# Kernel tuning notes

Hardware: AMD Instinct MI355X
Metric: run time of the kernel (lower is better)

## Reference

```python
import jax, jax.numpy as jnp
import numpy as np

N_NODES = 100000
N_EDGES = 800000
F_IN, HID, N_CLS = 256, 128, 32


def setup_inputs() -> dict:
    key = jax.random.key(0)
    k1, k2, k3, k4, k5 = jax.random.split(key, 5)
    features = jax.random.normal(k1, (N_NODES, F_IN), dtype=jnp.float32)
    # random directed edges with no self loops (so add_remaining_self_loops == append all loops)
    src = jax.random.randint(k2, (N_EDGES,), 0, N_NODES)
    off = jax.random.randint(k3, (N_EDGES,), 1, N_NODES)
    dst = (src + off) % N_NODES
    edge_index = jnp.stack([src, dst]).astype(jnp.int64)
    # Glorot-style params for the two GCNConv layers
    W1 = jax.random.normal(k4, (F_IN, HID), dtype=jnp.float32) * (1.0 / np.sqrt(F_IN))
    b1 = jnp.zeros((HID,), dtype=jnp.float32)
    W2 = jax.random.normal(k5, (HID, N_CLS), dtype=jnp.float32) * (1.0 / np.sqrt(HID))
    b2 = jnp.zeros((N_CLS,), dtype=jnp.float32)
    return {"features": features, "edge_index": edge_index, "W1": W1, "b1": b1, "W2": W2, "b2": b2}


def _gcn_conv(x, W, b, src, dst, norm, n):
    xw = x @ W                                  # [N, d_out] dense GEMM
    msg = xw[src] * norm[:, None]               # gather + scale, [E, d_out]
    out = jax.ops.segment_sum(msg, dst, num_segments=n)  # scatter-add to targets
    return out + b


def reference(features, edge_index, W1, b1, W2, b2):
    n = features.shape[0]
    # add_remaining_self_loops (input has none, so append all)
    loops = jnp.arange(n, dtype=edge_index.dtype)
    src = jnp.concatenate([edge_index[0], loops])
    dst = jnp.concatenate([edge_index[1], loops])
    # gcn_norm: deg over targets, sym normalization deg^-1/2 A deg^-1/2
    deg = jax.ops.segment_sum(jnp.ones_like(src, dtype=features.dtype), dst, num_segments=n)
    dinv = jnp.where(deg > 0, jax.lax.rsqrt(deg), 0.0)
    norm = dinv[src] * dinv[dst]
    x = _gcn_conv(features, W1, b1, src, dst, norm, n)
    x = jax.nn.relu(x)
    # dropout is identity at inference (training=False)
    x = _gcn_conv(x, W2, b2, src, dst, norm, n)
    return jax.nn.log_softmax(x, axis=1)
```

## Files before the change

### kernel.cpp

```cpp
#include <hip/hip_runtime.h>
#include <hip/hip_bf16.h>

typedef __bf16 bf16_t;
typedef __attribute__((ext_vector_type(8))) __bf16 bf16x8;
typedef __attribute__((ext_vector_type(4))) float f32x4;
typedef __attribute__((ext_vector_type(2))) float f32x2;

__device__ inline int xcc_id() {
    int x;
    asm volatile("s_getreg_b32 %0, hwreg(20, 0, 32)" : "=s"(x));
    return x & 7;
}
__device__ inline int l2AtomicAdd(int* p, int v) {
    return __hip_atomic_fetch_add(p, v, __ATOMIC_RELAXED, __HIP_MEMORY_SCOPE_WORKGROUP);
}

__device__ inline void packB_one(const float* __restrict__ B, bf16_t* __restrict__ Bp,
                                 int N, int idx) {
    int j    = idx & 7;
    int lane = (idx >> 3) & 63;
    int st   = idx >> 9;
    int nt   = N >> 4;
    int s = st / nt, t = st - s * nt;
    int k = s * 32 + (lane >> 4) * 8 + j;
    int n = t * 16 + (lane & 15);
    Bp[idx] = (bf16_t)B[(size_t)k * N + n];
}

__device__ inline void fma8_fp8(uint2 u, float w, float* a) {
    f32x2 p;
    p = __builtin_amdgcn_cvt_pk_f32_fp8(u.x, false); a[0] += p[0] * w; a[1] += p[1] * w;
    p = __builtin_amdgcn_cvt_pk_f32_fp8(u.x, true);  a[2] += p[0] * w; a[3] += p[1] * w;
    p = __builtin_amdgcn_cvt_pk_f32_fp8(u.y, false); a[4] += p[0] * w; a[5] += p[1] * w;
    p = __builtin_amdgcn_cvt_pk_f32_fp8(u.y, true);  a[6] += p[0] * w; a[7] += p[1] * w;
}

__global__ __launch_bounds__(256) void k_prep(
        const float* __restrict__ W1, bf16_t* __restrict__ Bp1,
        const float* __restrict__ W2, bf16_t* __restrict__ Bp2,
        int* __restrict__ deg8, int n8) {
    int b = blockIdx.x, t = threadIdx.x;
    const int PACKB = (32768 + 4096) / 256;
    if (b < PACKB) {
        int idx = b * 256 + t;
        if (idx < 32768) packB_one(W1, Bp1, 128, idx);
        else             packB_one(W2, Bp2, 32, idx - 32768);
        return;
    }
    int i = ((b - PACKB) * 256 + t) * 4;
    if (i < n8) {
        if (i + 4 <= n8) *(int4*)(deg8 + i) = make_int4(0, 0, 0, 0);
        else for (int j = 0; i + j < n8; ++j) deg8[i + j] = 0;
    }
}

template <int KSTEPS, int NTILES>
__global__ __launch_bounds__(256) void k_front(
        const float* __restrict__ feat, const bf16_t* __restrict__ Bp1,
        unsigned char* __restrict__ XW1, int M,
        const int* __restrict__ dst, int* __restrict__ deg8,
        int* __restrict__ rank, int Nn, int E, int DEGB) {
    int b = blockIdx.x, t = threadIdx.x;
    if (b < DEGB) {
        int x = xcc_id();
        int* degx = deg8 + (size_t)x * Nn;
        int tag = x << 28;
        int i = b * 1024 + t * 4;
        if (i + 4 <= E) {
            int4 v = *(const int4*)(dst + i);
            int4 r;
            r.x = l2AtomicAdd(&degx[v.x], 1) | tag;
            r.y = l2AtomicAdd(&degx[v.y], 1) | tag;
            r.z = l2AtomicAdd(&degx[v.z], 1) | tag;
            r.w = l2AtomicAdd(&degx[v.w], 1) | tag;
            *(int4*)(rank + i) = r;
        } else {
            for (int j = 0; j < 4; ++j)
                if (i + j < E) rank[i + j] = l2AtomicAdd(&degx[dst[i + j]], 1) | tag;
        }
        return;
    }
    b -= DEGB;
    {
        int wave = (b * 256 + t) >> 6;
        if (wave * 16 >= M) return;
        int lane = t & 63;
        int r16 = lane & 15, quad = lane >> 4;
        const int K = KSTEPS * 32, N = NTILES * 16;
        f32x4 acc[NTILES] = {};
        const float* arow = feat + (size_t)(wave * 16 + r16) * K + quad * 8;
#pragma unroll
        for (int s = 0; s < KSTEPS; ++s) {
            const float* ap = arow + s * 32;
            bf16x8 a;
#pragma unroll
            for (int j = 0; j < 8; ++j) a[j] = (bf16_t)ap[j];
            const bf16_t* bp = Bp1 + ((size_t)(s * NTILES) * 64 + lane) * 8;
#pragma unroll
            for (int tt = 0; tt < NTILES; ++tt) {
                bf16x8 bb = *(const bf16x8*)(bp + tt * 512);
                acc[tt] = __builtin_amdgcn_mfma_f32_16x16x32_bf16(a, bb, acc[tt], 0, 0, 0);
            }
        }
#pragma unroll
        for (int tt = 0; tt < NTILES; ++tt)
#pragma unroll
            for (int r = 0; r < 4; ++r) {
                int pk = __builtin_amdgcn_cvt_pk_fp8_f32(acc[tt][r], acc[tt][r], 0, false);
                XW1[(size_t)(wave * 16 + quad * 4 + r) * N + tt * 16 + r16] =
                    (unsigned char)pk;
            }
    }
}

__global__ __launch_bounds__(256) void k_dinv_scan1(
        const int* __restrict__ deg8, int* __restrict__ degTot,
        int* __restrict__ off, float* __restrict__ dinv,
        int* __restrict__ bsum, int n) {
    __shared__ int red[256];
    int b = blockIdx.x, t = threadIdx.x;
    int base = b * 1024 + t * 4;
    int s = 0;
#pragma unroll
    for (int j = 0; j < 4; ++j) {
        int i = base + j;
        if (i < n) {
            int run = 0;
#pragma unroll
            for (int x = 0; x < 8; ++x) {
                int v = deg8[(size_t)x * n + i];
                off[(size_t)x * n + i] = run;
                run += v;
            }
            degTot[i] = run;
            s += run;
            dinv[i] = rsqrtf((float)(run + 1));
        }
    }
    red[t] = s;
    __syncthreads();
    for (int d = 128; d > 0; d >>= 1) {
        if (t < d) red[t] += red[t + d];
        __syncthreads();
    }
    if (t == 0) bsum[b] = red[0];
}

__global__ __launch_bounds__(256) void k_scan3f(const int* __restrict__ degTot,
                                                const int* __restrict__ bsum, int nb,
                                                int* __restrict__ rowPtr, int n) {
    __shared__ int red[256];
    __shared__ int boff[256];
    int b = blockIdx.x, t = threadIdx.x;
    int base = b * 1024 + t * 4;
    int v[4]; int s = 0;
#pragma unroll
    for (int j = 0; j < 4; ++j) { int i = base + j; v[j] = (i < n) ? degTot[i] : 0; s += v[j]; }
    red[t] = s;
    boff[t] = (t < nb) ? bsum[t] : 0;
    __syncthreads();
    for (int d = 1; d < 256; d <<= 1) {
        int u  = (t >= d) ? red[t - d]  : 0;
        int u2 = (t >= d) ? boff[t - d] : 0;
        __syncthreads();
        red[t] += u;
        boff[t] += u2;
        __syncthreads();
    }
    int blockOff = (b == 0) ? 0 : boff[b - 1];
    if (b == 0 && t == 0) rowPtr[n] = boff[nb - 1];
    int run = blockOff + red[t] - s;
#pragma unroll
    for (int j = 0; j < 4; ++j) {
        int i = base + j;
        if (i < n) { rowPtr[i] = run; run += v[j]; }
    }
}

__global__ __launch_bounds__(256) void k_scatter(
        const int* __restrict__ src, const int* __restrict__ dst,
        const int* __restrict__ rank, const int* __restrict__ rowPtr,
        const int* __restrict__ off, const float* __restrict__ dinv,
        int2* __restrict__ edata, int Nn, int E) {
    int i = (blockIdx.x * 256 + threadIdx.x) * 4;
    if (i + 4 <= E) {
        int4 s4 = *(const int4*)(src + i);
        int4 d4 = *(const int4*)(dst + i);
        int4 r4 = *(const int4*)(rank + i);
        int p0 = rowPtr[d4.x] + off[(size_t)(((unsigned)r4.x) >> 28) * Nn + d4.x] + (r4.x & 0x0FFFFFFF);
        int p1 = rowPtr[d4.y] + off[(size_t)(((unsigned)r4.y) >> 28) * Nn + d4.y] + (r4.y & 0x0FFFFFFF);
        int p2 = rowPtr[d4.z] + off[(size_t)(((unsigned)r4.z) >> 28) * Nn + d4.z] + (r4.z & 0x0FFFFFFF);
        int p3 = rowPtr[d4.w] + off[(size_t)(((unsigned)r4.w) >> 28) * Nn + d4.w] + (r4.w & 0x0FFFFFFF);
        int2 e0; e0.x = s4.x; e0.y = __float_as_int(dinv[s4.x] * dinv[d4.x]);
        int2 e1; e1.x = s4.y; e1.y = __float_as_int(dinv[s4.y] * dinv[d4.y]);
        int2 e2; e2.x = s4.z; e2.y = __float_as_int(dinv[s4.z] * dinv[d4.z]);
        int2 e3; e3.x = s4.w; e3.y = __float_as_int(dinv[s4.w] * dinv[d4.w]);
        edata[p0] = e0; edata[p1] = e1; edata[p2] = e2; edata[p3] = e3;
    } else {
        for (int j = 0; j < 4; ++j) {
            int e = i + j;
            if (e >= E) break;
            int s = src[e], d = dst[e];
            int r = rank[e];
            int2 p; p.x = s; p.y = __float_as_int(dinv[s] * dinv[d]);
            edata[rowPtr[d] + off[(size_t)(((unsigned)r) >> 28) * Nn + d] + (r & 0x0FFFFFFF)] = p;
        }
    }
}

template <int KSTEPS, int NTILES>
__global__ __launch_bounds__(256) void k_gemm_p(
        const bf16_t* __restrict__ Ap, const bf16_t* __restrict__ Bp,
        bf16_t* __restrict__ C, int M) {
    int wave = (blockIdx.x * blockDim.x + threadIdx.x) >> 6;
    if (wave * 16 >= M) return;
    int lane = threadIdx.x & 63;
    int r16 = lane & 15, quad = lane >> 4;
    const int N = NTILES * 16;
    f32x4 acc[NTILES] = {};
    const bf16_t* apb = Ap + (size_t)wave * (KSTEPS * 512) + lane * 8;
#pragma unroll
    for (int s = 0; s < KSTEPS; ++s) {
        bf16x8 a = *(const bf16x8*)(apb + s * 512);
        const bf16_t* bp = Bp + ((size_t)(s * NTILES) * 64 + lane) * 8;
#pragma unroll
        for (int t = 0; t < NTILES; ++t) {
            bf16x8 b = *(const bf16x8*)(bp + t * 512);
            acc[t] = __builtin_amdgcn_mfma_f32_16x16x32_bf16(a, b, acc[t], 0, 0, 0);
        }
    }
#pragma unroll
    for (int t = 0; t < NTILES; ++t)
#pragma unroll
        for (int r = 0; r < 4; ++r)
            C[(size_t)(wave * 16 + quad * 4 + r) * N + t * 16 + r16] = (bf16_t)acc[t][r];
}

__global__ __launch_bounds__(256) void k_agg1(
        const int* __restrict__ rowPtr, const int2* __restrict__ edata,
        const unsigned char* __restrict__ XW1, const float* __restrict__ dinv,
        const float* __restrict__ b1, bf16_t* __restrict__ Hp, int n) {
    int wave = (blockIdx.x * blockDim.x + threadIdx.x) >> 6;
    if (wave >= n) return;
    int lane = threadIdx.x & 63;
    int fl = (lane & 15) << 3;
    int h  = lane >> 4;
    int r0 = rowPtr[wave], r1 = rowPtr[wave + 1];
    float d = dinv[wave], d2 = d * d;
    uint2 us = *(const uint2*)(XW1 + (size_t)wave * 128 + fl);
    float a0[8] = {}, a1[8] = {};
    int k = r0 + h;
    for (; k + 4 < r1; k += 8) {
        int2 e0 = edata[k], e1 = edata[k + 4];
        float w0 = __int_as_float(e0.y), w1 = __int_as_float(e1.y);
        uint2 u0 = *(const uint2*)(XW1 + (size_t)e0.x * 128 + fl);
        uint2 u1 = *(const uint2*)(XW1 + (size_t)e1.x * 128 + fl);
        fma8_fp8(u0, w0, a0);
        fma8_fp8(u1, w1, a1);
    }
    if (k < r1) {
        int2 e0 = edata[k];
        float w0 = __int_as_float(e0.y);
        uint2 u0 = *(const uint2*)(XW1 + (size_t)e0.x * 128 + fl);
        fma8_fp8(u0, w0, a0);
    }
#pragma unroll
    for (int j = 0; j < 8; ++j) {
        a0[j] += a1[j];
        a0[j] += __shfl_xor(a0[j], 16);
        a0[j] += __shfl_xor(a0[j], 32);
    }
    if (h == 0) {
        fma8_fp8(us, d2, a0);
        bf16x8 hv;
#pragma unroll
        for (int j = 0; j < 8; ++j) {
            float v = a0[j] + b1[fl + j];
            hv[j] = (bf16_t)fmaxf(v, 0.f);
        }
        int q = lane & 15;
        size_t off2 = (((size_t)(wave >> 4) * 4 + (q >> 2)) * 64
                       + (wave & 15) + 16 * (q & 3)) * 8;
        *(bf16x8*)(Hp + off2) = hv;
    }
}

__global__ __launch_bounds__(256) void k_agg2(
        const int* __restrict__ rowPtr, const int2* __restrict__ edata,
        const bf16_t* __restrict__ XW2, const float* __restrict__ dinv,
        const float* __restrict__ b2, float* __restrict__ out, int n) {
    int wave = (blockIdx.x * blockDim.x + threadIdx.x) >> 6;
    if (wave >= n) return;
    int lane = threadIdx.x & 63;
    int g = lane & 15;
    int h = lane >> 4;
    int r0 = rowPtr[wave], r1 = rowPtr[wave + 1];
    float d = dinv[wave], d2 = d * d;
    unsigned ps = *(const unsigned*)(XW2 + ((size_t)wave << 5) + 2 * g);
    float2 bb = *(const float2*)(b2 + 2 * g);
    float a00 = 0.f, a01 = 0.f, a10 = 0.f, a11 = 0.f;
    int k = r0 + h;
    for (; k + 4 < r1; k += 8) {
        int2 e0 = edata[k], e1 = edata[k + 4];
        float w0 = __int_as_float(e0.y), w1 = __int_as_float(e1.y);
        unsigned p0 = *(const unsigned*)(XW2 + ((size_t)e0.x << 5) + 2 * g);
        unsigned p1 = *(const unsigned*)(XW2 + ((size_t)e1.x << 5) + 2 * g);
        a00 += __int_as_float(p0 << 16) * w0;
        a01 += __int_as_float(p0 & 0xffff0000u) * w0;
        a10 += __int_as_float(p1 << 16) * w1;
        a11 += __int_as_float(p1 & 0xffff0000u) * w1;
    }
    if (k < r1) {
        int2 e0 = edata[k];
        float w0 = __int_as_float(e0.y);
        unsigned p0 = *(const unsigned*)(XW2 + ((size_t)e0.x << 5) + 2 * g);
        a00 += __int_as_float(p0 << 16) * w0;
        a01 += __int_as_float(p0 & 0xffff0000u) * w0;
    }
    float v0 = a00 + a10, v1 = a01 + a11;
    v0 += __shfl_xor(v0, 16); v0 += __shfl_xor(v0, 32);
    v1 += __shfl_xor(v1, 16); v1 += __shfl_xor(v1, 32);
    v0 += __int_as_float(ps << 16) * d2 + bb.x;
    v1 += __int_as_float(ps & 0xffff0000u) * d2 + bb.y;
    float mx = fmaxf(v0, v1);
#pragma unroll
    for (int m = 8; m >= 1; m >>= 1) mx = fmaxf(mx, __shfl_xor(mx, m));
    float s = __expf(v0 - mx) + __expf(v1 - mx);
#pragma unroll
    for (int m = 8; m >= 1; m >>= 1) s += __shfl_xor(s, m);
    if (h == 0) {
        float ls = __logf(s);
        float2 o; o.x = v0 - mx - ls; o.y = v1 - mx - ls;
        *(float2*)(out + ((size_t)wave << 5) + 2 * g) = o;
    }
}

extern "C" void kernel_launch(void* const* d_in, const int* in_sizes, int n_in,
                              void* d_out, int out_size, void* d_ws, size_t ws_size,
                              hipStream_t stream) {
    const float* feat = (const float*)d_in[0];
    const int*   eidx = (const int*)d_in[1];
    const float* W1   = (const float*)d_in[2];
    const float* b1   = (const float*)d_in[3];
    const float* W2   = (const float*)d_in[4];
    const float* b2   = (const float*)d_in[5];
    float* out = (float*)d_out;

    const int FIN = 256, HID = 128, NCLS = 32;
    const int N = in_sizes[0] / FIN;
    const int E = in_sizes[1] / 2;
    const int* src = eidx;
    const int* dst = eidx + E;

    char* ws = (char*)d_ws;
    size_t o = 0;
    auto alloc = [&](size_t bytes) -> void* {
        void* p = ws + o;
        o = (o + bytes + 255) & ~(size_t)255;
        return p;
    };
    int*    deg8   = (int*)   alloc((size_t)8 * N * 4);
    int*    offA   = (int*)   alloc((size_t)8 * N * 4);
    int*    degTot = (int*)   alloc((size_t)N * 4);
    int*    rank   = (int*)   alloc((size_t)E * 4);
    float*  dinv   = (float*) alloc((size_t)N * 4);
    int*    rowPtr = (int*)   alloc((size_t)(N + 1) * 4);
    int*    bsum   = (int*)   alloc(256 * 4);
    bf16_t* Bp1    = (bf16_t*)alloc((size_t)(FIN / 32) * (HID / 16) * 512 * 2);
    bf16_t* Bp2    = (bf16_t*)alloc((size_t)(HID / 32) * (NCLS / 16) * 512 * 2);
    int2*   edata  = (int2*)  alloc((size_t)E * 8);
    unsigned char* XW1 = (unsigned char*)alloc((size_t)N * HID);
    bf16_t* Hp     = (bf16_t*)alloc((size_t)N * HID * 2);
    bf16_t* XW2    = (bf16_t*)XW1;

    const int T = 256;
    const int NB = (N + 1023) >> 10;
    const int DEGB  = (E + 1023) / 1024;
    const int GEMMB = (((N + 15) / 16) * 64 + T - 1) / T;
    const int PACKB = (32768 + 4096) / 256;
    const int ZB    = (8 * N / 4 + T - 1) / T;

    k_prep      <<<PACKB + ZB, T, 0, stream>>>(W1, Bp1, W2, Bp2, deg8, 8 * N);
    k_front<8, 8><<<DEGB + GEMMB, T, 0, stream>>>(
        feat, Bp1, XW1, N, dst, deg8, rank, N, E, DEGB);
    k_dinv_scan1<<<NB, T, 0, stream>>>(deg8, degTot, offA, dinv, bsum, N);
    k_scan3f    <<<NB, T, 0, stream>>>(degTot, bsum, NB, rowPtr, N);
    k_scatter   <<<(E + 1023) / 1024, T, 0, stream>>>(
        src, dst, rank, rowPtr, offA, dinv, edata, N, E);
    k_agg1<<<(N * 64 + T - 1) / T, T, 0, stream>>>(rowPtr, edata, XW1, dinv, b1, Hp, N);
    {
        int waves = (N + 15) / 16;
        k_gemm_p<4, 2><<<(waves * 64 + T - 1) / T, T, 0, stream>>>(Hp, Bp2, XW2, N);
    }
    k_agg2<<<(N * 64 + T - 1) / T, T, 0, stream>>>(rowPtr, edata, XW2, dinv, b2, out, N);
}
```

Before: 323.1 us.

## Replace global per-XCC degree atomics with LDS range-partitioned histograms

The degree count now runs in 512 blocks, each owning one node range and one edge slice. Each block scans its slice of dst, counts edges whose target falls in its range with shared-memory atomics, and writes the counts to a per-slice plane. This replaces global atomics on per-XCC copies and removes the zeroing pass in k_prep. The cost is that every block reads its full edge slice, so the dst array is read once per range (32 times in total). The per-node offset planes also grow from 8 to 16 slices, which adds traffic to the scan and scatter kernels.

```diff
diff --git a/kernel.cpp b/kernel.cpp
--- a/kernel.cpp
+++ b/kernel.cpp
@@ -6,14 +6,8 @@
 typedef __attribute__((ext_vector_type(4))) float f32x4;
 typedef __attribute__((ext_vector_type(2))) float f32x2;
 
-__device__ inline int xcc_id() {
-    int x;
-    asm volatile("s_getreg_b32 %0, hwreg(20, 0, 32)" : "=s"(x));
-    return x & 7;
-}
-__device__ inline int l2AtomicAdd(int* p, int v) {
-    return __hip_atomic_fetch_add(p, v, __ATOMIC_RELAXED, __HIP_MEMORY_SCOPE_WORKGROUP);
-}
+#define RANGES 32
+#define SLICES 16
 
 __device__ inline void packB_one(const float* __restrict__ B, bf16_t* __restrict__ Bp,
                                  int N, int idx) {
@@ -37,47 +31,49 @@
 
 __global__ __launch_bounds__(256) void k_prep(
         const float* __restrict__ W1, bf16_t* __restrict__ Bp1,
-        const float* __restrict__ W2, bf16_t* __restrict__ Bp2,
-        int* __restrict__ deg8, int n8) {
-    int b = blockIdx.x, t = threadIdx.x;
-    const int PACKB = (32768 + 4096) / 256;
-    if (b < PACKB) {
-        int idx = b * 256 + t;
-        if (idx < 32768) packB_one(W1, Bp1, 128, idx);
-        else             packB_one(W2, Bp2, 32, idx - 32768);
-        return;
-    }
-    int i = ((b - PACKB) * 256 + t) * 4;
-    if (i < n8) {
-        if (i + 4 <= n8) *(int4*)(deg8 + i) = make_int4(0, 0, 0, 0);
-        else for (int j = 0; i + j < n8; ++j) deg8[i + j] = 0;
-    }
+        const float* __restrict__ W2, bf16_t* __restrict__ Bp2) {
+    int idx = blockIdx.x * 256 + threadIdx.x;
+    if (idx < 32768) packB_one(W1, Bp1, 128, idx);
+    else             packB_one(W2, Bp2, 32, idx - 32768);
 }
 
 template <int KSTEPS, int NTILES>
 __global__ __launch_bounds__(256) void k_front(
         const float* __restrict__ feat, const bf16_t* __restrict__ Bp1,
         unsigned char* __restrict__ XW1, int M,
-        const int* __restrict__ dst, int* __restrict__ deg8,
+        const int* __restrict__ dst, int* __restrict__ degS,
         int* __restrict__ rank, int Nn, int E, int DEGB) {
     int b = blockIdx.x, t = threadIdx.x;
     if (b < DEGB) {
-        int x = xcc_id();
-        int* degx = deg8 + (size_t)x * Nn;
-        int tag = x << 28;
-        int i = b * 1024 + t * 4;
-        if (i + 4 <= E) {
-            int4 v = *(const int4*)(dst + i);
-            int4 r;
-            r.x = l2AtomicAdd(&degx[v.x], 1) | tag;
-            r.y = l2AtomicAdd(&degx[v.y], 1) | tag;
-            r.z = l2AtomicAdd(&degx[v.z], 1) | tag;
-            r.w = l2AtomicAdd(&degx[v.w], 1) | tag;
-            *(int4*)(rank + i) = r;
-        } else {
-            for (int j = 0; j < 4; ++j)
-                if (i + j < E) rank[i + j] = l2AtomicAdd(&degx[dst[i + j]], 1) | tag;
-        }
+        __shared__ int hist[3200];
+        const int CHUNK = (Nn + RANGES - 1) / RANGES;
+        int r = b >> 4, s = b & (SLICES - 1);
+        int base = r * CHUNK;
+        int top  = min(base + CHUNK, Nn);
+        int len  = top - base;
+        for (int i = t; i < len; i += 256) hist[i] = 0;
+        __syncthreads();
+        int tag = s << 24;
+        int sliceLen = ((E + (SLICES * 4 - 1)) / (SLICES * 4)) * 4;
+        int e0 = s * sliceLen;
+        int e1 = min(e0 + sliceLen, E);
+        for (int i = e0 + t * 4; i < e1; i += 1024) {
+            if (i + 4 <= e1) {
+                int4 v = *(const int4*)(dst + i);
+                if (v.x >= base && v.x < top) rank[i]     = tag | atomicAdd(&hist[v.x - base], 1);
+                if (v.y >= base && v.y < top) rank[i + 1] = tag | atomicAdd(&hist[v.y - base], 1);
+                if (v.z >= base && v.z < top) rank[i + 2] = tag | atomicAdd(&hist[v.z - base], 1);
+                if (v.w >= base && v.w < top) rank[i + 3] = tag | atomicAdd(&hist[v.w - base], 1);
+            } else {
+                for (int j = 0; j < 4 && i + j < e1; ++j) {
+                    int d = dst[i + j];
+                    if (d >= base && d < top) rank[i + j] = tag | atomicAdd(&hist[d - base], 1);
+                }
+            }
+        }
+        __syncthreads();
+        int* dplane = degS + (size_t)s * Nn + base;
+        for (int i = t; i < len; i += 256) dplane[i] = hist[i];
         return;
     }
     b -= DEGB;
@@ -114,7 +110,7 @@
 }
 
 __global__ __launch_bounds__(256) void k_dinv_scan1(
-        const int* __restrict__ deg8, int* __restrict__ degTot,
+        const int* __restrict__ degS, int* __restrict__ degTot,
         int* __restrict__ off, float* __restrict__ dinv,
         int* __restrict__ bsum, int n) {
     __shared__ int red[256];
@@ -127,8 +123,8 @@
         if (i < n) {
             int run = 0;
 #pragma unroll
-            for (int x = 0; x < 8; ++x) {
-                int v = deg8[(size_t)x * n + i];
+            for (int x = 0; x < SLICES; ++x) {
+                int v = degS[(size_t)x * n + i];
                 off[(size_t)x * n + i] = run;
                 run += v;
             }
@@ -187,10 +183,10 @@
         int4 s4 = *(const int4*)(src + i);
         int4 d4 = *(const int4*)(dst + i);
         int4 r4 = *(const int4*)(rank + i);
-        int p0 = rowPtr[d4.x] + off[(size_t)(((unsigned)r4.x) >> 28) * Nn + d4.x] + (r4.x & 0x0FFFFFFF);
-        int p1 = rowPtr[d4.y] + off[(size_t)(((unsigned)r4.y) >> 28) * Nn + d4.y] + (r4.y & 0x0FFFFFFF);
-        int p2 = rowPtr[d4.z] + off[(size_t)(((unsigned)r4.z) >> 28) * Nn + d4.z] + (r4.z & 0x0FFFFFFF);
-        int p3 = rowPtr[d4.w] + off[(size_t)(((unsigned)r4.w) >> 28) * Nn + d4.w] + (r4.w & 0x0FFFFFFF);
+        int p0 = rowPtr[d4.x] + off[(size_t)(((unsigned)r4.x) >> 24) * Nn + d4.x] + (r4.x & 0x00FFFFFF);
+        int p1 = rowPtr[d4.y] + off[(size_t)(((unsigned)r4.y) >> 24) * Nn + d4.y] + (r4.y & 0x00FFFFFF);
+        int p2 = rowPtr[d4.z] + off[(size_t)(((unsigned)r4.z) >> 24) * Nn + d4.z] + (r4.z & 0x00FFFFFF);
+        int p3 = rowPtr[d4.w] + off[(size_t)(((unsigned)r4.w) >> 24) * Nn + d4.w] + (r4.w & 0x00FFFFFF);
         int2 e0; e0.x = s4.x; e0.y = __float_as_int(dinv[s4.x] * dinv[d4.x]);
         int2 e1; e1.x = s4.y; e1.y = __float_as_int(dinv[s4.y] * dinv[d4.y]);
         int2 e2; e2.x = s4.z; e2.y = __float_as_int(dinv[s4.z] * dinv[d4.z]);
@@ -203,7 +199,7 @@
             int s = src[e], d = dst[e];
             int r = rank[e];
             int2 p; p.x = s; p.y = __float_as_int(dinv[s] * dinv[d]);
-            edata[rowPtr[d] + off[(size_t)(((unsigned)r) >> 28) * Nn + d] + (r & 0x0FFFFFFF)] = p;
+            edata[rowPtr[d] + off[(size_t)(((unsigned)r) >> 24) * Nn + d] + (r & 0x00FFFFFF)] = p;
         }
     }
 }
@@ -359,8 +355,8 @@
         o = (o + bytes + 255) & ~(size_t)255;
         return p;
     };
-    int*    deg8   = (int*)   alloc((size_t)8 * N * 4);
-    int*    offA   = (int*)   alloc((size_t)8 * N * 4);
+    int*    degS   = (int*)   alloc((size_t)SLICES * N * 4);
+    int*    offA   = (int*)   alloc((size_t)SLICES * N * 4);
     int*    degTot = (int*)   alloc((size_t)N * 4);
     int*    rank   = (int*)   alloc((size_t)E * 4);
     float*  dinv   = (float*) alloc((size_t)N * 4);
@@ -375,15 +371,14 @@
 
     const int T = 256;
     const int NB = (N + 1023) >> 10;
-    const int DEGB  = (E + 1023) / 1024;
+    const int DEGB  = RANGES * SLICES;
     const int GEMMB = (((N + 15) / 16) * 64 + T - 1) / T;
     const int PACKB = (32768 + 4096) / 256;
-    const int ZB    = (8 * N / 4 + T - 1) / T;
-
-    k_prep      <<<PACKB + ZB, T, 0, stream>>>(W1, Bp1, W2, Bp2, deg8, 8 * N);
+
+    k_prep      <<<PACKB, T, 0, stream>>>(W1, Bp1, W2, Bp2);
     k_front<8, 8><<<DEGB + GEMMB, T, 0, stream>>>(
-        feat, Bp1, XW1, N, dst, deg8, rank, N, E, DEGB);
-    k_dinv_scan1<<<NB, T, 0, stream>>>(deg8, degTot, offA, dinv, bsum, N);
+        feat, Bp1, XW1, N, dst, degS, rank, N, E, DEGB);
+    k_dinv_scan1<<<NB, T, 0, stream>>>(degS, degTot, offA, dinv, bsum, N);
     k_scan3f    <<<NB, T, 0, stream>>>(degTot, bsum, NB, rowPtr, N);
     k_scatter   <<<(E + 1023) / 1024, T, 0, stream>>>(
         src, dst, rank, rowPtr, offA, dinv, edata, N, E);
```

New measurement: 311.6 us. 3.6% less time.
